# Performance work log

Measured on AMD Instinct MI355X. Metric: run time of the kernel, lower is better.

Reference implementation:

```python
import jax, jax.numpy as jnp
from jax import lax
import numpy as np

B, S, D = 32, 2048, 512

def setup_inputs() -> dict:
    key = jax.random.key(0)
    ks = jax.random.split(key, 9)
    inv = 1.0 / np.sqrt(D).astype(np.float32)
    return {
        "query": jax.random.normal(ks[0], (B, 1, D), jnp.float32),
        "value": jax.random.normal(ks[1], (B, S, D), jnp.float32),
        "last_alignment_energy": jax.random.uniform(ks[2], (B, S), jnp.float32),
        "conv_w": jax.random.normal(ks[3], (D, 1, 3), jnp.float32) * 0.1,  # Conv1d(1->D,k=3)
        "conv_b": jax.random.normal(ks[4], (D,), jnp.float32) * 0.01,
        "w_q": jax.random.normal(ks[5], (D, D), jnp.float32) * inv,  # applied as x @ w_q
        "w_v": jax.random.normal(ks[6], (D, D), jnp.float32) * inv,
        "bias": jax.random.uniform(ks[7], (D,), jnp.float32, minval=-0.1, maxval=0.1),
        "score_w": jax.random.normal(ks[8], (D,), jnp.float32) * inv,  # score_proj weight (out=1)
        "score_b": jnp.zeros((), jnp.float32),
    }


def reference(query, value, last_alignment_energy, conv_w, conv_b, w_q, w_v, bias, score_w, score_b):
    # location features: Conv1d(1->D, k=3, pad=1) over the previous alignment
    loc = lax.conv_general_dilated(
        last_alignment_energy[:, None, :], conv_w,
        window_strides=(1,), padding=[(1, 1)],
        dimension_numbers=("NCH", "OIH", "NCH"))  # [B, D, S]
    loc = jnp.transpose(loc, (0, 2, 1)) + conv_b  # [B, S, D]

    # additive attention energy: tanh(Wq q + Wv v + loc + b) @ score_w
    hidden = jnp.tanh(query @ w_q + value @ w_v + loc + bias)  # [B, S, D] (query broadcasts over S)
    scores = hidden @ score_w + score_b                          # [B, S]
    align = jax.nn.softmax(scores, axis=-1)                      # [B, S]

    # context = align^T V
    context = jnp.einsum("bs,bsd->bd", align, value)             # [B, D]
    return context, align
```

## Files before the change

kernel.cpp:

```cpp
#include <hip/hip_runtime.h>
#include <hip/hip_bf16.h>

#define B_ 32
#define S_ 2048
#define D_ 512
#define M_ (B_*S_)

typedef __bf16 bf16x8 __attribute__((ext_vector_type(8)));
typedef float  f32x4  __attribute__((ext_vector_type(4)));

__device__ __forceinline__ float tanh_fast(float x){
  float e2 = __expf(2.f * x);
  return 1.f - 2.f * __builtin_amdgcn_rcpf(e2 + 1.f);
}

__global__ void k_reorder_wv(const float* __restrict__ wv,
                             unsigned short* __restrict__ wvr){
  int frag = blockIdx.x;
  int lane = threadIdx.x;
  int ks = frag >> 5, nt = frag & 31;
  int k0 = ks*32 + (lane>>4)*8;
  int d  = nt*16 + (lane&15);
  bf16x8 t;
  #pragma unroll
  for (int j=0;j<8;++j) t[j] = (__bf16)wv[(k0+j)*D_ + d];
  *reinterpret_cast<uint4*>(wvr + ((size_t)frag*64 + lane)*8) =
      __builtin_bit_cast(uint4, t);
}

__global__ void k_qproj(const float* __restrict__ q,
                        const float* __restrict__ wq,
                        const float* __restrict__ bias,
                        float* __restrict__ qp){
  int b  = blockIdx.y;
  int t  = threadIdx.x;
  int dl = t & 127, eg = t >> 7;
  int d  = blockIdx.x*128 + dl;
  __shared__ float qs[D_];
  __shared__ float red[4][128];
  for (int e=t; e<D_; e+=512) qs[e] = q[b*D_+e];
  __syncthreads();
  float acc = 0.f;
  #pragma unroll 8
  for (int i=0;i<128;++i){
    int e = eg*128 + i;
    acc = fmaf(qs[e], wq[(size_t)e*D_+d], acc);
  }
  red[eg][dl] = acc;
  __syncthreads();
  if (eg == 0)
    qp[b*D_+d] = red[0][dl]+red[1][dl]+red[2][dl]+red[3][dl] + bias[d];
}

__launch_bounds__(256, 2)
__global__ void k_energy(const float* __restrict__ value,
                         const unsigned short* __restrict__ wvr,
                         const float* __restrict__ qp,
                         const float* __restrict__ energy,
                         const float* __restrict__ conv_w,
                         const float* __restrict__ conv_b,
                         const float* __restrict__ score_w,
                         float* __restrict__ scores){
  const int t    = threadIdx.x;
  const int wave = t >> 6;
  const int lane = t & 63;
  const int quad = lane >> 4;
  const int lm   = lane & 15;
  const int row0 = blockIdx.x * 64;
  const int b    = row0 >> 11;
  const int s0   = row0 & (S_-1);

  __shared__ __align__(16) unsigned short As[2][4][64][8];

  const int sr  = t >> 2;
  const int so  = t & 3;
  const float* gA = value + (size_t)(row0+sr)*D_ + so*8;
  unsigned short* wA = &As[0][sr>>4][so*16 + (sr&15)][0];

  f32x4 acc[4][8];
  #pragma unroll
  for (int mt=0;mt<4;++mt)
    #pragma unroll
    for (int nt=0;nt<8;++nt)
      acc[mt][nt] = (f32x4){0.f,0.f,0.f,0.f};

  const unsigned short* bP = wvr + ((size_t)(wave*8)*64 + lane)*8;

  {
    f32x4 p0 = *reinterpret_cast<const f32x4*>(gA);
    f32x4 p1 = *reinterpret_cast<const f32x4*>(gA+4);
    bf16x8 tt;
    tt[0]=(__bf16)p0[0]; tt[1]=(__bf16)p0[1]; tt[2]=(__bf16)p0[2]; tt[3]=(__bf16)p0[3];
    tt[4]=(__bf16)p1[0]; tt[5]=(__bf16)p1[1]; tt[6]=(__bf16)p1[2]; tt[7]=(__bf16)p1[3];
    *reinterpret_cast<uint4*>(wA) = __builtin_bit_cast(uint4, tt);
  }
  __syncthreads();

  for (int kc=0; kc<16; ++kc){
    const int buf = kc & 1;
    f32x4 n0, n1;
    if (kc < 15){
      n0 = *reinterpret_cast<const f32x4*>(gA + (kc+1)*32);
      n1 = *reinterpret_cast<const f32x4*>(gA + (kc+1)*32 + 4);
    }
    bf16x8 a[4];
    #pragma unroll
    for (int mt=0;mt<4;++mt)
      a[mt] = *reinterpret_cast<const bf16x8*>(&As[buf][mt][lane][0]);
    bf16x8 bfr[8];
    #pragma unroll
    for (int ntl=0;ntl<8;++ntl)
      bfr[ntl] = __builtin_bit_cast(bf16x8,
        *reinterpret_cast<const uint4*>(bP + (size_t)(kc*32+ntl)*64*8));
    #pragma unroll
    for (int ntl=0;ntl<8;++ntl)
      #pragma unroll
      for (int mt=0;mt<4;++mt)
        acc[mt][ntl] = __builtin_amdgcn_mfma_f32_16x16x32_bf16(a[mt], bfr[ntl], acc[mt][ntl], 0,0,0);
    if (kc < 15){
      bf16x8 tt;
      tt[0]=(__bf16)n0[0]; tt[1]=(__bf16)n0[1]; tt[2]=(__bf16)n0[2]; tt[3]=(__bf16)n0[3];
      tt[4]=(__bf16)n1[0]; tt[5]=(__bf16)n1[1]; tt[6]=(__bf16)n1[2]; tt[7]=(__bf16)n1[3];
      *reinterpret_cast<uint4*>(wA + (buf^1)*2048) = __builtin_bit_cast(uint4, tt);
    }
    __syncthreads();
  }

  float sw[8], c0[8], c1[8], c2[8], cb[8], qv[8];
  #pragma unroll
  for (int ntl=0; ntl<8; ++ntl){
    int d = wave*128 + ntl*16 + lm;
    sw[ntl] = score_w[d];
    c0[ntl] = conv_w[d*3+0];
    c1[ntl] = conv_w[d*3+1];
    c2[ntl] = conv_w[d*3+2];
    cb[ntl] = conv_b[d];
    qv[ntl] = qp[b*D_+d];
  }
  float* red = (float*)&As[0][0][0][0];
  const float* eB = energy + b*S_;
  #pragma unroll
  for (int mt=0; mt<4; ++mt){
    #pragma unroll
    for (int r=0;r<4;++r){
      int sl = mt*16 + quad*4 + r;
      int s  = s0 + sl;
      float em1 = (s > 0)    ? eB[s-1] : 0.f;
      float e0  =              eB[s];
      float ep1 = (s < S_-1) ? eB[s+1] : 0.f;
      float p = 0.f;
      #pragma unroll
      for (int ntl=0; ntl<8; ++ntl){
        float h = acc[mt][ntl][r] + qv[ntl]
                + fmaf(c0[ntl],em1, fmaf(c1[ntl],e0, fmaf(c2[ntl],ep1, cb[ntl])));
        p = fmaf(sw[ntl], tanh_fast(h), p);
      }
      #pragma unroll
      for (int m=1; m<16; m<<=1) p += __shfl_xor(p, m, 64);
      if (lm == 0) red[wave*64 + sl] = p;
    }
  }
  __syncthreads();
  if (t < 64)
    scores[row0 + t] = red[t] + red[64+t] + red[128+t] + red[192+t];
}

__global__ void k_softmax(const float* __restrict__ sp,
                          const float* __restrict__ score_b,
                          float* __restrict__ out_align){
  int b = blockIdx.x, t = threadIdx.x;
  int lane = t & 63, wid = t >> 6;
  float sb = score_b[0];
  float v[8], mx = -3.4e38f;
  #pragma unroll
  for (int i=0;i<8;++i){
    float sc = sp[b*S_ + t + i*256] + sb;
    v[i] = sc;
    mx = fmaxf(mx, sc);
  }
  __shared__ float red[4], red2[4];
  #pragma unroll
  for (int m=1;m<64;m<<=1) mx = fmaxf(mx, __shfl_xor(mx, m, 64));
  if (lane==0) red[wid] = mx;
  __syncthreads();
  mx = fmaxf(fmaxf(red[0],red[1]), fmaxf(red[2],red[3]));
  float sum = 0.f;
  #pragma unroll
  for (int i=0;i<8;++i){ v[i] = __expf(v[i]-mx); sum += v[i]; }
  #pragma unroll
  for (int m=1;m<64;m<<=1) sum += __shfl_xor(sum, m, 64);
  if (lane==0) red2[wid] = sum;
  __syncthreads();
  sum = red2[0]+red2[1]+red2[2]+red2[3];
  float inv = 1.f/sum;
  #pragma unroll
  for (int i=0;i<8;++i) out_align[b*S_ + t + i*256] = v[i]*inv;
}

__global__ void k_ctx_part(const float* __restrict__ value,
                           const float* __restrict__ align,
                           float* __restrict__ cpart){
  int b = blockIdx.y, sc = blockIdx.x;
  int t = threadIdx.x;
  int r = t >> 7;
  int c = (t & 127) * 4;
  f32x4 acc = (f32x4){0.f,0.f,0.f,0.f};
  for (int i=0;i<64;++i){
    int s = sc*128 + i*2 + r;
    float al = align[b*S_+s];
    f32x4 v = *reinterpret_cast<const f32x4*>(value + ((size_t)(b*S_+s))*D_ + c);
    acc += al * v;
  }
  __shared__ float lred[2][D_];
  #pragma unroll
  for (int j=0;j<4;++j) lred[r][c+j] = acc[j];
  __syncthreads();
  if (r == 0){
    #pragma unroll
    for (int j=0;j<4;++j)
      cpart[((size_t)(b*16+sc))*D_ + c + j] = lred[0][c+j] + lred[1][c+j];
  }
}

__global__ void k_ctx_reduce(const float* __restrict__ cpart,
                             float* __restrict__ out_ctx){
  int idx = blockIdx.x*256 + threadIdx.x;
  int b = idx >> 9, d = idx & 511;
  float s = 0.f;
  #pragma unroll
  for (int j=0;j<16;++j) s += cpart[((size_t)(b*16+j))*D_ + d];
  out_ctx[idx] = s;
}

extern "C" void kernel_launch(void* const* d_in, const int* in_sizes, int n_in,
                              void* d_out, int out_size, void* d_ws, size_t ws_size,
                              hipStream_t stream){
  const float* query   = (const float*)d_in[0];
  const float* value   = (const float*)d_in[1];
  const float* energy  = (const float*)d_in[2];
  const float* conv_w  = (const float*)d_in[3];
  const float* conv_b  = (const float*)d_in[4];
  const float* w_q     = (const float*)d_in[5];
  const float* w_v     = (const float*)d_in[6];
  const float* bias    = (const float*)d_in[7];
  const float* score_w = (const float*)d_in[8];
  const float* score_b = (const float*)d_in[9];

  char* ws = (char*)d_ws;
  unsigned short* wvr = (unsigned short*)(ws);
  float* qp    = (float*)(ws + (512<<10));
  float* sp    = (float*)(ws + (576<<10));
  float* cpart = (float*)(ws + (832<<10));

  float* out_ctx   = (float*)d_out;
  float* out_align = out_ctx + B_*D_;

  k_reorder_wv<<<dim3(512),      dim3(64),  0, stream>>>(w_v, wvr);
  k_qproj     <<<dim3(4,32),     dim3(512), 0, stream>>>(query, w_q, bias, qp);
  k_energy    <<<dim3(M_/64),    dim3(256), 0, stream>>>(value, wvr, qp, energy,
                                                         conv_w, conv_b, score_w, sp);
  k_softmax   <<<dim3(B_),       dim3(256), 0, stream>>>(sp, score_b, out_align);
  k_ctx_part  <<<dim3(16,B_),    dim3(256), 0, stream>>>(value, out_align, cpart);
  k_ctx_reduce<<<dim3(B_*D_/256),dim3(256), 0, stream>>>(cpart, out_ctx);
}
```

Measured before the change: 286.5 us.

## Deepen energy GEMM K-step with register-prefetched B fragments; split context over more blocks

```diff
diff --git a/kernel.cpp b/kernel.cpp
--- a/kernel.cpp
+++ b/kernel.cpp
@@ -12,6 +12,13 @@
 __device__ __forceinline__ float tanh_fast(float x){
   float e2 = __expf(2.f * x);
   return 1.f - 2.f * __builtin_amdgcn_rcpf(e2 + 1.f);
+}
+
+__device__ __forceinline__ uint4 cvt8(f32x4 p0, f32x4 p1){
+  bf16x8 tt;
+  tt[0]=(__bf16)p0[0]; tt[1]=(__bf16)p0[1]; tt[2]=(__bf16)p0[2]; tt[3]=(__bf16)p0[3];
+  tt[4]=(__bf16)p1[0]; tt[5]=(__bf16)p1[1]; tt[6]=(__bf16)p1[2]; tt[7]=(__bf16)p1[3];
+  return __builtin_bit_cast(uint4, tt);
 }
 
 __global__ void k_reorder_wv(const float* __restrict__ wv,
@@ -70,12 +77,12 @@
   const int b    = row0 >> 11;
   const int s0   = row0 & (S_-1);
 
-  __shared__ __align__(16) unsigned short As[2][4][64][8];
+  __shared__ __align__(16) unsigned short As[2][2][4][64][8];
 
   const int sr  = t >> 2;
   const int so  = t & 3;
   const float* gA = value + (size_t)(row0+sr)*D_ + so*8;
-  unsigned short* wA = &As[0][sr>>4][so*16 + (sr&15)][0];
+  unsigned short* wA = &As[0][0][sr>>4][so*16 + (sr&15)][0];
 
   f32x4 acc[4][8];
   #pragma unroll
@@ -86,42 +93,73 @@
 
   const unsigned short* bP = wvr + ((size_t)(wave*8)*64 + lane)*8;
 
+  bf16x8 bcur[8], bnxt[8];
+  #pragma unroll
+  for (int n=0;n<8;++n)
+    bcur[n] = __builtin_bit_cast(bf16x8,
+        *reinterpret_cast<const uint4*>(bP + (size_t)n*512));
   {
     f32x4 p0 = *reinterpret_cast<const f32x4*>(gA);
-    f32x4 p1 = *reinterpret_cast<const f32x4*>(gA+4);
-    bf16x8 tt;
-    tt[0]=(__bf16)p0[0]; tt[1]=(__bf16)p0[1]; tt[2]=(__bf16)p0[2]; tt[3]=(__bf16)p0[3];
-    tt[4]=(__bf16)p1[0]; tt[5]=(__bf16)p1[1]; tt[6]=(__bf16)p1[2]; tt[7]=(__bf16)p1[3];
-    *reinterpret_cast<uint4*>(wA) = __builtin_bit_cast(uint4, tt);
-  }
-  __syncthreads();
-
-  for (int kc=0; kc<16; ++kc){
-    const int buf = kc & 1;
-    f32x4 n0, n1;
-    if (kc < 15){
-      n0 = *reinterpret_cast<const f32x4*>(gA + (kc+1)*32);
-      n1 = *reinterpret_cast<const f32x4*>(gA + (kc+1)*32 + 4);
-    }
-    bf16x8 a[4];
+    f32x4 p1 = *reinterpret_cast<const f32x4*>(gA + 4);
+    f32x4 p2 = *reinterpret_cast<const f32x4*>(gA + 32);
+    f32x4 p3 = *reinterpret_cast<const f32x4*>(gA + 36);
+    *reinterpret_cast<uint4*>(wA)        = cvt8(p0, p1);
+    *reinterpret_cast<uint4*>(wA + 2048) = cvt8(p2, p3);
+  }
+  __syncthreads();
+
+  for (int p=0; p<8; ++p){
+    const int buf = p & 1;
+    unsigned short* wAp = wA + (buf^1)*4096;
+
+    f32x4 n0, n1, n2, n3;
+    if (p < 7){
+      const float* g = gA + (p+1)*64;
+      n0 = *reinterpret_cast<const f32x4*>(g);
+      n1 = *reinterpret_cast<const f32x4*>(g + 4);
+      n2 = *reinterpret_cast<const f32x4*>(g + 32);
+      n3 = *reinterpret_cast<const f32x4*>(g + 36);
+    }
+
     #pragma unroll
-    for (int mt=0;mt<4;++mt)
-      a[mt] = *reinterpret_cast<const bf16x8*>(&As[buf][mt][lane][0]);
-    bf16x8 bfr[8];
-    #pragma unroll
-    for (int ntl=0;ntl<8;++ntl)
-      bfr[ntl] = __builtin_bit_cast(bf16x8,
-        *reinterpret_cast<const uint4*>(bP + (size_t)(kc*32+ntl)*64*8));
-    #pragma unroll
-    for (int ntl=0;ntl<8;++ntl)
+    for (int n=0;n<8;++n)
+      bnxt[n] = __builtin_bit_cast(bf16x8,
+          *reinterpret_cast<const uint4*>(bP + (size_t)((2*p+1)*32+n)*512));
+
+    {
+      bf16x8 a[4];
       #pragma unroll
       for (int mt=0;mt<4;++mt)
-        acc[mt][ntl] = __builtin_amdgcn_mfma_f32_16x16x32_bf16(a[mt], bfr[ntl], acc[mt][ntl], 0,0,0);
-    if (kc < 15){
-      bf16x8 tt;
-      tt[0]=(__bf16)n0[0]; tt[1]=(__bf16)n0[1]; tt[2]=(__bf16)n0[2]; tt[3]=(__bf16)n0[3];
-      tt[4]=(__bf16)n1[0]; tt[5]=(__bf16)n1[1]; tt[6]=(__bf16)n1[2]; tt[7]=(__bf16)n1[3];
-      *reinterpret_cast<uint4*>(wA + (buf^1)*2048) = __builtin_bit_cast(uint4, tt);
+        a[mt] = *reinterpret_cast<const bf16x8*>(&As[buf][0][mt][lane][0]);
+      #pragma unroll
+      for (int ntl=0;ntl<8;++ntl)
+        #pragma unroll
+        for (int mt=0;mt<4;++mt)
+          acc[mt][ntl] = __builtin_amdgcn_mfma_f32_16x16x32_bf16(a[mt], bnxt[0]*0.f==bnxt[0]*0.f ? bcur[ntl] : bcur[ntl], acc[mt][ntl], 0,0,0);
+    }
+
+    if (p < 7){
+      #pragma unroll
+      for (int n=0;n<8;++n)
+        bcur[n] = __builtin_bit_cast(bf16x8,
+            *reinterpret_cast<const uint4*>(bP + (size_t)((2*p+2)*32+n)*512));
+    }
+
+    {
+      bf16x8 a[4];
+      #pragma unroll
+      for (int mt=0;mt<4;++mt)
+        a[mt] = *reinterpret_cast<const bf16x8*>(&As[buf][1][mt][lane][0]);
+      #pragma unroll
+      for (int ntl=0;ntl<8;++ntl)
+        #pragma unroll
+        for (int mt=0;mt<4;++mt)
+          acc[mt][ntl] = __builtin_amdgcn_mfma_f32_16x16x32_bf16(a[mt], bnxt[ntl], acc[mt][ntl], 0,0,0);
+    }
+
+    if (p < 7){
+      *reinterpret_cast<uint4*>(wAp)        = cvt8(n0, n1);
+      *reinterpret_cast<uint4*>(wAp + 2048) = cvt8(n2, n3);
     }
     __syncthreads();
   }
@@ -137,7 +175,7 @@
     cb[ntl] = conv_b[d];
     qv[ntl] = qp[b*D_+d];
   }
-  float* red = (float*)&As[0][0][0][0];
+  float* red = (float*)&As[0][0][0][0][0];
   const float* eB = energy + b*S_;
   #pragma unroll
   for (int mt=0; mt<4; ++mt){
@@ -204,12 +242,15 @@
   int t = threadIdx.x;
   int r = t >> 7;
   int c = (t & 127) * 4;
+  __shared__ float al[64];
+  if (t < 64) al[t] = align[b*S_ + sc*64 + t];
+  __syncthreads();
   f32x4 acc = (f32x4){0.f,0.f,0.f,0.f};
-  for (int i=0;i<64;++i){
-    int s = sc*128 + i*2 + r;
-    float al = align[b*S_+s];
-    f32x4 v = *reinterpret_cast<const f32x4*>(value + ((size_t)(b*S_+s))*D_ + c);
-    acc += al * v;
+  const float* vbase = value + ((size_t)(b*S_ + sc*64 + r))*D_ + c;
+  #pragma unroll 8
+  for (int i=0;i<32;++i){
+    f32x4 v = *reinterpret_cast<const f32x4*>(vbase + (size_t)(2*i)*D_);
+    acc += al[2*i+r] * v;
   }
   __shared__ float lred[2][D_];
   #pragma unroll
@@ -218,7 +259,7 @@
   if (r == 0){
     #pragma unroll
     for (int j=0;j<4;++j)
-      cpart[((size_t)(b*16+sc))*D_ + c + j] = lred[0][c+j] + lred[1][c+j];
+      cpart[((size_t)(b*32+sc))*D_ + c + j] = lred[0][c+j] + lred[1][c+j];
   }
 }
 
@@ -228,7 +269,7 @@
   int b = idx >> 9, d = idx & 511;
   float s = 0.f;
   #pragma unroll
-  for (int j=0;j<16;++j) s += cpart[((size_t)(b*16+j))*D_ + d];
+  for (int j=0;j<32;++j) s += cpart[((size_t)(b*32+j))*D_ + d];
   out_ctx[idx] = s;
 }
 
@@ -260,6 +301,6 @@
   k_energy    <<<dim3(M_/64),    dim3(256), 0, stream>>>(value, wvr, qp, energy,
                                                          conv_w, conv_b, score_w, sp);
   k_softmax   <<<dim3(B_),       dim3(256), 0, stream>>>(sp, score_b, out_align);
-  k_ctx_part  <<<dim3(16,B_),    dim3(256), 0, stream>>>(value, out_align, cpart);
+  k_ctx_part  <<<dim3(32,B_),    dim3(256), 0, stream>>>(value, out_align, cpart);
   k_ctx_reduce<<<dim3(B_*D_/256),dim3(256), 0, stream>>>(cpart, out_ctx);
 }
```

Result: faster. 271.3 us (-5.3%).
